# Kernel optimization log

Measured on AMD Instinct MI355X. Metric: run time of the kernel, lower is better.

## Reference

```python
import jax, jax.numpy as jnp
import numpy as np
from jax import lax

B, C, H, W = 8, 256, 64, 64
HEADS = 8
STRIDE = 2


def _grouped_conv(x, w, b, stride, groups):
    # x: [B, Cin, H, W]; w: [Cout, Cin/groups, k, k] (OIHW)
    y = lax.conv_general_dilated(x, w, (stride, stride), 'VALID',
                                 dimension_numbers=('NCHW', 'OIHW', 'NCHW'),
                                 feature_group_count=groups)
    return y + b[None, :, None, None]


def _grouped_conv_transpose(x, w, b, stride, groups):
    # Equivalent of torch ConvTranspose2d(kernel=stride, stride=stride, groups=groups)
    # implemented as lhs-dilated conv. w: [Cout, Cin/groups, k, k] (already in conv-equivalent layout).
    k = w.shape[-1]
    pad = k - 1
    y = lax.conv_general_dilated(x, w, (1, 1), [(pad, pad), (pad, pad)],
                                 lhs_dilation=(stride, stride),
                                 dimension_numbers=('NCHW', 'OIHW', 'NCHW'),
                                 feature_group_count=groups)
    return y + b[None, :, None, None]


def setup_inputs() -> dict:
    key = jax.random.key(0)
    ks = jax.random.split(key, 12)
    s = 0.05
    inp = {
        'q': jax.random.normal(ks[0], (B, C, H, W), jnp.float32),
        'k': jax.random.normal(ks[1], (B, C, H, W), jnp.float32),
        'v': jax.random.normal(ks[2], (B, C, H, W), jnp.float32),
        # grouped QKV conv weights: groups=C, out=C*HEADS -> [C*HEADS, 1, s, s]
        'wq': jax.random.normal(ks[3], (C * HEADS, 1, STRIDE, STRIDE), jnp.float32) * s,
        'bq': jax.random.normal(ks[4], (C * HEADS,), jnp.float32) * s,
        'wk': jax.random.normal(ks[5], (C * HEADS, 1, STRIDE, STRIDE), jnp.float32) * s,
        'bk': jax.random.normal(ks[6], (C * HEADS,), jnp.float32) * s,
        'wv': jax.random.normal(ks[7], (C * HEADS, 1, STRIDE, STRIDE), jnp.float32) * s,
        'bv': jax.random.normal(ks[8], (C * HEADS,), jnp.float32) * s,
        # deconv (groups=C, in=C*HEADS, out=C) in conv-equivalent OIHW layout: [C, HEADS, s, s]
        'wo': jax.random.normal(ks[9], (C, HEADS, STRIDE, STRIDE), jnp.float32) * s,
        'bo': jax.random.normal(ks[10], (C,), jnp.float32) * s,
        'gamma': jax.random.normal(ks[11], (1,), jnp.float32),
    }
    return inp


def reference(q, k, v, wq, bq, wk, bk, wv, bv, wo, bo, gamma):
    Bn, Cq, Hq, Wsp = q.shape
    Ckv = k.shape[1]
    # grouped conv projections -> [B, heads, C, L]
    pq = _grouped_conv(q, wq, bq, STRIDE, Cq).reshape(Bn, HEADS, Cq, -1)
    pk = _grouped_conv(k, wk, bk, STRIDE, Ckv).reshape(Bn, HEADS, Ckv, -1)
    pv = _grouped_conv(v, wv, bv, STRIDE, Ckv).reshape(Bn, HEADS, Ckv, -1)
    scale = pq.shape[3] ** (-0.5)
    # channel-wise attention: [B, h, Cq, Ckv]
    attn = jax.nn.softmax(jnp.einsum('bhcl,bhdl->bhcd', pq, pk) * scale, axis=-1)
    out = jnp.einsum('bhcd,bhdl->bhcl', attn, pv)  # [B, h, Cq, L]
    out = out.reshape(Bn, HEADS * Cq, Hq // STRIDE, Wsp // STRIDE)
    out = _grouped_conv_transpose(out, wo, bo, STRIDE, Cq)  # [B, Cq, Hq, Wsp]
    # dropout is identity at inference
    return q + out * gamma
```

## Files before the change

kernel.cpp:

```cpp
#include <hip/hip_runtime.h>
#include <hip/hip_bf16.h>

typedef __bf16 bf16;
typedef __bf16 bf16x4 __attribute__((ext_vector_type(4)));
typedef __bf16 bf16x8 __attribute__((ext_vector_type(8)));
typedef float f32x4 __attribute__((ext_vector_type(4)));

__device__ __forceinline__ void gload16(const void* g, void* l) {
  __builtin_amdgcn_global_load_lds(
      (const __attribute__((address_space(1))) unsigned int*)g,
      (__attribute__((address_space(3))) unsigned int*)l, 16, 0, 0);
}


__global__ __launch_bounds__(256) void proj_kqv(
    const float* __restrict__ kin, const float* __restrict__ qin,
    const float* __restrict__ vin,
    const float* __restrict__ wk, const float* __restrict__ bk,
    const float* __restrict__ wq, const float* __restrict__ bq,
    const float* __restrict__ wv, const float* __restrict__ bv,
    bf16* __restrict__ Pk, bf16* __restrict__ Pq, bf16* __restrict__ Vt) {
  int b = blockIdx.y;
  int x = blockIdx.x;
  int t = threadIdx.x;
  __shared__ float ch[4288];
  if (x < 512) {
    int g = x & 255;
    const float* in   = (x < 256) ? kin : qin;
    const float* w    = (x < 256) ? wk : wq;
    const float* bias = (x < 256) ? bk : bq;
    bf16* out         = (x < 256) ? Pk : Pq;
    {
      const float4* src = reinterpret_cast<const float4*>(in + ((size_t)b*256 + g)*4096);
      float4* dst4 = reinterpret_cast<float4*>(ch);
#pragma unroll
      for (int i = 0; i < 4; i++) dst4[t + i*256] = src[t + i*256];
    }
    int wave = t >> 6;
    int j = (t >> 3) & 7, n = t & 7;
    float4 wvv = reinterpret_cast<const float4*>(w)[g*8 + j];
    float bj = bias[g*8 + j];
    __syncthreads();
    int h = g >> 5;
    int c0 = (g & 31)*8;
    int bh = b*8 + h;
#pragma unroll
    for (int p = 0; p < 4; p++) {
      int kb = p*4 + wave;
      int m = kb*2 + (n >> 2);
      int n0 = (n & 3)*8;
      float rr0[16], rr1[16];
      const float4* R0 = reinterpret_cast<const float4*>(ch + (2*m)*64 + 2*n0);
      const float4* R1 = reinterpret_cast<const float4*>(ch + (2*m+1)*64 + 2*n0);
#pragma unroll
      for (int u = 0; u < 4; u++) {
        *reinterpret_cast<float4*>(rr0 + u*4) = R0[u];
        *reinterpret_cast<float4*>(rr1 + u*4) = R1[u];
      }
      bf16x8 o;
#pragma unroll
      for (int u = 0; u < 8; u++)
        o[u] = (bf16)(bj + wvv.x*rr0[2*u] + wvv.y*rr0[2*u+1] + wvv.z*rr1[2*u] + wvv.w*rr1[2*u+1]);
      size_t off = (((size_t)bh*16 + kb)*256 + c0 + j)*64 + (size_t)((n ^ j)*8);
      *reinterpret_cast<bf16x8*>(out + off) = o;
    }
  } else {
    int r = x - 512;
    int m = r & 31, h = r >> 5;
    {
      int seg = t >> 2, part = t & 3;
      int gl = seg >> 1, ky = seg & 1;
      const float* src = vin + (((size_t)b*256 + h*32 + gl)*64 + (2*m + ky))*64;
      float* drow = ch + (gl*2 + ky)*67;
#pragma unroll
      for (int i = 0; i < 4; i++) {
        float4 v = reinterpret_cast<const float4*>(src)[part + i*4];
        int x0 = (part + i*4)*4;
        drow[x0]=v.x; drow[x0+1]=v.y; drow[x0+2]=v.z; drow[x0+3]=v.w;
      }
    }
    int cgrp = t & 31, lgr = t >> 5;
    int c0 = cgrp*8;
    float4 wv8[8]; float bb8[8];
#pragma unroll
    for (int u = 0; u < 8; u++) {
      wv8[u] = reinterpret_cast<const float4*>(wv)[h*256 + c0 + u];
      bb8[u] = bv[h*256 + c0 + u];
    }
    __syncthreads();
    const float* r0 = ch + (cgrp*2 + 0)*67;
    const float* r1 = ch + (cgrp*2 + 1)*67;
    int bh = b*8 + h;
    bf16* base = Vt + ((size_t)bh*4 + (c0 >> 6))*1024*64;
    int colx = (c0 & 63) ^ (lgr << 3);
#pragma unroll
    for (int p = 0; p < 4; p++) {
      int n = p*8 + lgr;
      int l = m*32 + n;
      float c00 = r0[2*n], c01 = r0[2*n+1], c10 = r1[2*n], c11 = r1[2*n+1];
      bf16x8 o;
#pragma unroll
      for (int u = 0; u < 8; u++)
        o[u] = (bf16)(bb8[u] + wv8[u].x*c00 + wv8[u].y*c01 + wv8[u].z*c10 + wv8[u].w*c11);
      *reinterpret_cast<bf16x8*>(base + (size_t)l*64 + colx) = o;
    }
  }
}

__global__ __launch_bounds__(256, 2) void attn_qk(
    const bf16* __restrict__ Pq, const bf16* __restrict__ Pk,
    bf16* __restrict__ Pattn) {
  int raw = blockIdx.x;
  int idx = raw >> 3;
  int bh = (raw & 7)*8 + (idx >> 2);
  int cs = idx & 3;
  int t = threadIdx.x, wave = t >> 6, lane = t & 63, lg = lane >> 4, lr = lane & 15;
  __shared__ __attribute__((aligned(16))) char smem[81920];
  bf16* Kb0 = reinterpret_cast<bf16*>(smem);
  bf16* Kb1 = reinterpret_cast<bf16*>(smem + 32768);
  bf16* Qb0 = reinterpret_cast<bf16*>(smem + 65536);
  bf16* Qb1 = reinterpret_cast<bf16*>(smem + 73728);
  float (*red)[64] = reinterpret_cast<float (*)[64]>(smem + 65536);
  bf16* Pst = reinterpret_cast<bf16*>(smem);
  const char* Kbase = (const char*)Pk + (size_t)bh*524288 + wave*8192 + lane*16;
  const char* Qbase = (const char*)Pq + (size_t)bh*524288 + (size_t)cs*8192 + wave*2048 + lane*16;
  char* Kd0 = (char*)Kb0 + wave*8192;  char* Kd1 = (char*)Kb1 + wave*8192;
  char* Qd0 = (char*)Qb0 + wave*2048;  char* Qd1 = (char*)Qb1 + wave*2048;

#define STAGE(kb, K_, Q_) { \
    const char* kc = Kbase + (size_t)(kb)*32768; \
    _Pragma("unroll") \
    for (int i_ = 0; i_ < 8; i_++) gload16(kc + i_*1024, (K_) + i_*1024); \
    const char* qc = Qbase + (size_t)(kb)*32768; \
    gload16(qc, (Q_)); gload16(qc + 1024, (Q_) + 1024); }

  f32x4 acc[4][4];
#pragma unroll
  for (int i = 0; i < 4; i++)
#pragma unroll
    for (int j = 0; j < 4; j++) { f32x4 z = {0.f,0.f,0.f,0.f}; acc[i][j] = z; }

  STAGE(0, Kd0, Qd0);
#pragma unroll
  for (int kb = 0; kb < 16; kb++) {
    if (kb < 15) {
      if (kb & 1) { STAGE(kb+1, Kd0, Qd0); } else { STAGE(kb+1, Kd1, Qd1); }
      asm volatile("s_waitcnt vmcnt(10)" ::: "memory");
    } else {
      asm volatile("s_waitcnt vmcnt(0)" ::: "memory");
    }
    __builtin_amdgcn_s_barrier();
    __builtin_amdgcn_sched_barrier(0);
    const bf16* Kc = (kb & 1) ? Kb1 : Kb0;
    const bf16* Qc = (kb & 1) ? Qb1 : Qb0;
#pragma unroll
    for (int ks = 0; ks < 2; ks++) {
      int colx = (ks*32 + lg*8) ^ ((lr & 7) << 3);
      bf16x8 a[4];
#pragma unroll
      for (int mi = 0; mi < 4; mi++)
        a[mi] = *reinterpret_cast<const bf16x8*>(Qc + (mi*16 + lr)*64 + colx);
#pragma unroll
      for (int ni = 0; ni < 4; ni++) {
        bf16x8 bv2 = *reinterpret_cast<const bf16x8*>(Kc + (wave*64 + ni*16 + lr)*64 + colx);
#pragma unroll
        for (int mi = 0; mi < 4; mi++)
          acc[mi][ni] = __builtin_amdgcn_mfma_f32_16x16x32_bf16(a[mi], bv2, acc[mi][ni], 0, 0, 0);
      }
    }
    __builtin_amdgcn_s_barrier();
    __builtin_amdgcn_sched_barrier(0);
  }
#undef STAGE
  const float scale = 0.03125f;
  float sums[4][4];
#pragma unroll
  for (int mi = 0; mi < 4; mi++)
#pragma unroll
    for (int r = 0; r < 4; r++) {
      float mx = fmaxf(fmaxf(acc[mi][0][r], acc[mi][1][r]), fmaxf(acc[mi][2][r], acc[mi][3][r]));
#pragma unroll
      for (int off = 1; off < 16; off <<= 1) mx = fmaxf(mx, __shfl_xor(mx, off, 64));
      red[wave][mi*16 + lg*4 + r] = mx;
    }
  __syncthreads();
#pragma unroll
  for (int mi = 0; mi < 4; mi++)
#pragma unroll
    for (int r = 0; r < 4; r++) {
      int clr = mi*16 + lg*4 + r;
      float mx = fmaxf(fmaxf(red[0][clr], red[1][clr]), fmaxf(red[2][clr], red[3][clr]));
      float s = 0.f;
#pragma unroll
      for (int ni = 0; ni < 4; ni++) {
        float p = __expf(scale*(acc[mi][ni][r] - mx));
        acc[mi][ni][r] = p; s += p;
      }
#pragma unroll
      for (int off = 1; off < 16; off <<= 1) s += __shfl_xor(s, off, 64);
      sums[mi][r] = s;
    }
  __syncthreads();
#pragma unroll
  for (int mi = 0; mi < 4; mi++)
#pragma unroll
    for (int r = 0; r < 4; r++) red[wave][mi*16 + lg*4 + r] = sums[mi][r];
  __syncthreads();
#pragma unroll
  for (int mi = 0; mi < 4; mi++)
#pragma unroll
    for (int r = 0; r < 4; r++) {
      int clr = mi*16 + lg*4 + r;
      float iv = 1.f/(red[0][clr] + red[1][clr] + red[2][clr] + red[3][clr]);
#pragma unroll
      for (int ni = 0; ni < 4; ni++) {
        int dl = ni*16 + lr;
        Pst[wave*4096 + clr*64 + (dl ^ ((clr & 7) << 3))] = (bf16)(acc[mi][ni][r]*iv);
      }
    }
  __syncthreads();
  const uint4* ls = reinterpret_cast<const uint4*>(Pst);
#pragma unroll
  for (int i = 0; i < 8; i++) {
    int f = i*256 + t;
    int kb = f >> 9, rem = f & 511;
    char* dst = (char*)Pattn + ((size_t)(bh*4 + kb)*256 + cs*64)*128 + (size_t)rem*16;
    *reinterpret_cast<uint4*>(dst) = ls[f];
  }
}

__global__ __launch_bounds__(256, 4) void pv_deconv(const bf16* __restrict__ Pattn,
    const bf16* __restrict__ Vt, const float* __restrict__ qin,
    const float* __restrict__ wo, const float* __restrict__ bo,
    const float* __restrict__ gamma, float* __restrict__ outp) {
  int raw = blockIdx.x;
  int idx = raw >> 3;
  int pair = (raw & 7)*32 + (idx >> 2);
  int tb = idx & 3;
  int mb = pair & 3, bh = pair >> 2;
  int h = bh & 7, b = bh >> 3;
  int t = threadIdx.x, wave = t >> 6, lane = t & 63, lg = lane >> 4, lr = lane & 15;
  __shared__ __attribute__((aligned(16))) char smem[40960];
  bf16* Pl   = reinterpret_cast<bf16*>(smem);
  bf16* Vl   = reinterpret_cast<bf16*>(smem + 8192);
  bf16* OlT  = reinterpret_cast<bf16*>(smem);
  float* wo_s = reinterpret_cast<float*>(smem + 36864);
  float* bo_s = reinterpret_cast<float*>(smem + 37888);
  const char* Pbase = (const char*)Pattn + ((size_t)bh*4*256 + tb*64)*128;
  const char* Vbase = (const char*)Vt + ((size_t)bh*4*1024 + mb*256)*128;
  f32x4 acc[4][4];
#pragma unroll
  for (int i = 0; i < 4; i++)
#pragma unroll
    for (int j = 0; j < 4; j++) { f32x4 z = {0.f,0.f,0.f,0.f}; acc[i][j] = z; }
  for (int kb = 0; kb < 4; kb++) {
    __syncthreads();
    {
      const char* pc = Pbase + (size_t)kb*32768 + wave*2048 + lane*16;
      char* pl = (char*)Pl + wave*2048;
#pragma unroll
      for (int i = 0; i < 2; i++) gload16(pc + i*1024, pl + i*1024);
      const char* vc = Vbase + (size_t)kb*131072 + wave*8192 + lane*16;
      char* vl = (char*)Vl + wave*8192;
#pragma unroll
      for (int i = 0; i < 8; i++) gload16(vc + i*1024, vl + i*1024);
    }
    __syncthreads();
#pragma unroll
    for (int ks = 0; ks < 2; ks++) {
      int colx = (ks*32 + lg*8) ^ ((lr & 7) << 3);
      bf16x8 a[4];
#pragma unroll
      for (int mi = 0; mi < 4; mi++)
        a[mi] = *reinterpret_cast<const bf16x8*>(Pl + (mi*16 + lr)*64 + colx);
#pragma unroll
      for (int ni = 0; ni < 4; ni++) {
        bf16x8 bv2 = *reinterpret_cast<const bf16x8*>(Vl + (wave*64 + ni*16 + lr)*64 + colx);
#pragma unroll
        for (int mi = 0; mi < 4; mi++)
          acc[mi][ni] = __builtin_amdgcn_mfma_f32_16x16x32_bf16(a[mi], bv2, acc[mi][ni], 0, 0, 0);
      }
    }
  }
  __syncthreads();
#pragma unroll
  for (int mi = 0; mi < 4; mi++)
#pragma unroll
    for (int ni = 0; ni < 4; ni++) {
      int l = wave*64 + ni*16 + lr;
      int cb = mi*16 + lg*4;
      bf16x4 p;
      p[0] = (bf16)acc[mi][ni][0]; p[1] = (bf16)acc[mi][ni][1];
      p[2] = (bf16)acc[mi][ni][2]; p[3] = (bf16)acc[mi][ni][3];
      *reinterpret_cast<bf16x4*>(OlT + l*66 + cb) = p;
    }
  wo_s[t] = wo[((size_t)(h*32 + tb*8 + (t>>5)))*32 + (t & 31)];
  if (t < 8) bo_s[t] = bo[h*32 + tb*8 + t];
  __syncthreads();
  int xq = t & 15, b5 = (t >> 4) & 1, ct = t >> 5;
  float2 wp[8];
#pragma unroll
  for (int j = 0; j < 8; j++)
    wp[j] = *reinterpret_cast<const float2*>(wo_s + ct*32 + j*4 + (1 - b5)*2);
  float bias = bo_s[ct];
  float gm = gamma[0];
  int co = h*32 + tb*8 + ct;
#pragma unroll
  for (int it = 0; it < 8; it++) {
    int y = it*2 + b5;
    int ll0 = it*32 + xq*2;
    bf16x4 o00 = *reinterpret_cast<const bf16x4*>(OlT + ll0*66 + ct*8);
    bf16x4 o01 = *reinterpret_cast<const bf16x4*>(OlT + ll0*66 + ct*8 + 4);
    bf16x4 o10 = *reinterpret_cast<const bf16x4*>(OlT + (ll0+1)*66 + ct*8);
    bf16x4 o11 = *reinterpret_cast<const bf16x4*>(OlT + (ll0+1)*66 + ct*8 + 4);
    float v0 = bias, v1 = bias, v2 = bias, v3 = bias;
#pragma unroll
    for (int j = 0; j < 4; j++) {
      float f0 = (float)o00[j], f1 = (float)o01[j];
      v0 += f0*wp[j].y;   v1 += f0*wp[j].x;
      v0 += f1*wp[4+j].y; v1 += f1*wp[4+j].x;
      float g0 = (float)o10[j], g1 = (float)o11[j];
      v2 += g0*wp[j].y;   v3 += g0*wp[j].x;
      v2 += g1*wp[4+j].y; v3 += g1*wp[4+j].x;
    }
    size_t oi = (((size_t)b*256 + co)*64 + (mb*16 + y))*64 + xq*4;
    float4 qv = *reinterpret_cast<const float4*>(qin + oi);
    float4 ov;
    ov.x = qv.x + gm*v0; ov.y = qv.y + gm*v1;
    ov.z = qv.z + gm*v2; ov.w = qv.w + gm*v3;
    *reinterpret_cast<float4*>(outp + oi) = ov;
  }
}

extern "C" void kernel_launch(void* const* d_in, const int* in_sizes, int n_in,
                              void* d_out, int out_size, void* d_ws, size_t ws_size,
                              hipStream_t stream) {
  const float* q  = (const float*)d_in[0];
  const float* k  = (const float*)d_in[1];
  const float* v  = (const float*)d_in[2];
  const float* wq = (const float*)d_in[3];
  const float* bq = (const float*)d_in[4];
  const float* wk = (const float*)d_in[5];
  const float* bk = (const float*)d_in[6];
  const float* wv = (const float*)d_in[7];
  const float* bv = (const float*)d_in[8];
  const float* wo = (const float*)d_in[9];
  const float* bo = (const float*)d_in[10];
  const float* gamma = (const float*)d_in[11];
  float* out = (float*)d_out;

  char* ws = (char*)d_ws;
  bf16* Pk    = (bf16*)(ws);
  bf16* Vt    = (bf16*)(ws + 33554432);
  bf16* Pattn = (bf16*)(ws + 67108864);
  bf16* Pq    = (bf16*)(ws + 75497472);

  proj_kqv<<<dim3(768, 8), 256, 0, stream>>>(k, q, v, wk, bk, wq, bq, wv, bv, Pk, Pq, Vt);
  attn_qk <<<dim3(256), 256, 0, stream>>>(Pq, Pk, Pattn);
  pv_deconv<<<dim3(1024), 256, 0, stream>>>(Pattn, Vt, q, wo, bo, gamma, out);
}
```

Measured before the change: 81.79 us.

## Fuse Q projection into attention QK kernel, drop Pq intermediate buffer

```diff
diff --git a/kernel.cpp b/kernel.cpp
--- a/kernel.cpp
+++ b/kernel.cpp
@@ -13,33 +13,27 @@
 }
 
 
-__global__ __launch_bounds__(256) void proj_kqv(
-    const float* __restrict__ kin, const float* __restrict__ qin,
-    const float* __restrict__ vin,
+__global__ __launch_bounds__(256) void proj_kv(
+    const float* __restrict__ kin, const float* __restrict__ vin,
     const float* __restrict__ wk, const float* __restrict__ bk,
-    const float* __restrict__ wq, const float* __restrict__ bq,
     const float* __restrict__ wv, const float* __restrict__ bv,
-    bf16* __restrict__ Pk, bf16* __restrict__ Pq, bf16* __restrict__ Vt) {
+    bf16* __restrict__ Pk, bf16* __restrict__ Vt) {
   int b = blockIdx.y;
   int x = blockIdx.x;
   int t = threadIdx.x;
   __shared__ float ch[4288];
-  if (x < 512) {
-    int g = x & 255;
-    const float* in   = (x < 256) ? kin : qin;
-    const float* w    = (x < 256) ? wk : wq;
-    const float* bias = (x < 256) ? bk : bq;
-    bf16* out         = (x < 256) ? Pk : Pq;
+  if (x < 256) {
+    int g = x;
     {
-      const float4* src = reinterpret_cast<const float4*>(in + ((size_t)b*256 + g)*4096);
+      const float4* src = reinterpret_cast<const float4*>(kin + ((size_t)b*256 + g)*4096);
       float4* dst4 = reinterpret_cast<float4*>(ch);
 #pragma unroll
       for (int i = 0; i < 4; i++) dst4[t + i*256] = src[t + i*256];
     }
     int wave = t >> 6;
     int j = (t >> 3) & 7, n = t & 7;
-    float4 wvv = reinterpret_cast<const float4*>(w)[g*8 + j];
-    float bj = bias[g*8 + j];
+    float4 wvv = reinterpret_cast<const float4*>(wk)[g*8 + j];
+    float bj = bk[g*8 + j];
     __syncthreads();
     int h = g >> 5;
     int c0 = (g & 31)*8;
@@ -62,10 +56,10 @@
       for (int u = 0; u < 8; u++)
         o[u] = (bf16)(bj + wvv.x*rr0[2*u] + wvv.y*rr0[2*u+1] + wvv.z*rr1[2*u] + wvv.w*rr1[2*u+1]);
       size_t off = (((size_t)bh*16 + kb)*256 + c0 + j)*64 + (size_t)((n ^ j)*8);
-      *reinterpret_cast<bf16x8*>(out + off) = o;
+      *reinterpret_cast<bf16x8*>(Pk + off) = o;
     }
   } else {
-    int r = x - 512;
+    int r = x - 256;
     int m = r & 31, h = r >> 5;
     {
       int seg = t >> 2, part = t & 3;
@@ -107,13 +101,15 @@
   }
 }
 
-__global__ __launch_bounds__(256, 2) void attn_qk(
-    const bf16* __restrict__ Pq, const bf16* __restrict__ Pk,
+__global__ __launch_bounds__(256, 2) void attn_fused(
+    const float* __restrict__ qraw, const float* __restrict__ wq,
+    const float* __restrict__ bq, const bf16* __restrict__ Pk,
     bf16* __restrict__ Pattn) {
   int raw = blockIdx.x;
   int idx = raw >> 3;
   int bh = (raw & 7)*8 + (idx >> 2);
   int cs = idx & 3;
+  int b = bh >> 3, h = bh & 7;
   int t = threadIdx.x, wave = t >> 6, lane = t & 63, lg = lane >> 4, lr = lane & 15;
   __shared__ __attribute__((aligned(16))) char smem[81920];
   bf16* Kb0 = reinterpret_cast<bf16*>(smem);
@@ -123,31 +119,72 @@
   float (*red)[64] = reinterpret_cast<float (*)[64]>(smem + 65536);
   bf16* Pst = reinterpret_cast<bf16*>(smem);
   const char* Kbase = (const char*)Pk + (size_t)bh*524288 + wave*8192 + lane*16;
-  const char* Qbase = (const char*)Pq + (size_t)bh*524288 + (size_t)cs*8192 + wave*2048 + lane*16;
   char* Kd0 = (char*)Kb0 + wave*8192;  char* Kd1 = (char*)Kb1 + wave*8192;
-  char* Qd0 = (char*)Qb0 + wave*2048;  char* Qd1 = (char*)Qb1 + wave*2048;
-
-#define STAGE(kb, K_, Q_) { \
+
+  int gg = 2*wave + (lane >> 5);
+  int j  = (lane >> 2) & 7;
+  int nq = lane & 3;
+  int g  = h*32 + cs*8 + gg;
+  const float* qch = qraw + ((size_t)b*256 + g)*4096;
+  float4 wvq = reinterpret_cast<const float4*>(wq)[g*8 + j];
+  float bj = bq[g*8 + j];
+  int x0 = nq*16;
+  bf16x8 qreg[16][2];
+#pragma unroll
+  for (int kb = 0; kb < 16; kb++) {
+#pragma unroll
+    for (int half = 0; half < 2; half++) {
+      int y0 = kb*4 + half*2;
+      const float4* R0 = reinterpret_cast<const float4*>(qch + y0*64 + x0);
+      const float4* R1 = reinterpret_cast<const float4*>(qch + (y0+1)*64 + x0);
+      float f0[16], f1[16];
+#pragma unroll
+      for (int u = 0; u < 4; u++) {
+        *reinterpret_cast<float4*>(f0 + u*4) = R0[u];
+        *reinterpret_cast<float4*>(f1 + u*4) = R1[u];
+      }
+      bf16x8 o;
+#pragma unroll
+      for (int u = 0; u < 8; u++)
+        o[u] = (bf16)(bj + wvq.x*f0[2*u] + wvq.y*f0[2*u+1] + wvq.z*f1[2*u] + wvq.w*f1[2*u+1]);
+      qreg[kb][half] = o;
+    }
+  }
+  int qrow = gg*8 + j;
+  bf16* qw0a = Qb0 + qrow*64 + ((nq     ^ j)*8);
+  bf16* qw0b = Qb0 + qrow*64 + (((4+nq) ^ j)*8);
+  bf16* qw1a = Qb1 + qrow*64 + ((nq     ^ j)*8);
+  bf16* qw1b = Qb1 + qrow*64 + (((4+nq) ^ j)*8);
+
+#define STAGEK(kb, K_) { \
     const char* kc = Kbase + (size_t)(kb)*32768; \
     _Pragma("unroll") \
-    for (int i_ = 0; i_ < 8; i_++) gload16(kc + i_*1024, (K_) + i_*1024); \
-    const char* qc = Qbase + (size_t)(kb)*32768; \
-    gload16(qc, (Q_)); gload16(qc + 1024, (Q_) + 1024); }
+    for (int i_ = 0; i_ < 8; i_++) gload16(kc + i_*1024, (K_) + i_*1024); }
 
   f32x4 acc[4][4];
 #pragma unroll
   for (int i = 0; i < 4; i++)
 #pragma unroll
-    for (int j = 0; j < 4; j++) { f32x4 z = {0.f,0.f,0.f,0.f}; acc[i][j] = z; }
-
-  STAGE(0, Kd0, Qd0);
+    for (int jj = 0; jj < 4; jj++) { f32x4 z = {0.f,0.f,0.f,0.f}; acc[i][jj] = z; }
+
+  *reinterpret_cast<bf16x8*>(qw0a) = qreg[0][0];
+  *reinterpret_cast<bf16x8*>(qw0b) = qreg[0][1];
+  STAGEK(0, Kd0);
 #pragma unroll
   for (int kb = 0; kb < 16; kb++) {
     if (kb < 15) {
-      if (kb & 1) { STAGE(kb+1, Kd0, Qd0); } else { STAGE(kb+1, Kd1, Qd1); }
-      asm volatile("s_waitcnt vmcnt(10)" ::: "memory");
+      if (kb & 1) {
+        STAGEK(kb+1, Kd0);
+        *reinterpret_cast<bf16x8*>(qw0a) = qreg[kb+1][0];
+        *reinterpret_cast<bf16x8*>(qw0b) = qreg[kb+1][1];
+      } else {
+        STAGEK(kb+1, Kd1);
+        *reinterpret_cast<bf16x8*>(qw1a) = qreg[kb+1][0];
+        *reinterpret_cast<bf16x8*>(qw1b) = qreg[kb+1][1];
+      }
+      asm volatile("s_waitcnt vmcnt(8) lgkmcnt(0)" ::: "memory");
     } else {
-      asm volatile("s_waitcnt vmcnt(0)" ::: "memory");
+      asm volatile("s_waitcnt vmcnt(0) lgkmcnt(0)" ::: "memory");
     }
     __builtin_amdgcn_s_barrier();
     __builtin_amdgcn_sched_barrier(0);
@@ -171,7 +208,7 @@
     __builtin_amdgcn_s_barrier();
     __builtin_amdgcn_sched_barrier(0);
   }
-#undef STAGE
+#undef STAGEK
   const float scale = 0.03125f;
   float sums[4][4];
 #pragma unroll
@@ -353,9 +390,8 @@
   bf16* Pk    = (bf16*)(ws);
   bf16* Vt    = (bf16*)(ws + 33554432);
   bf16* Pattn = (bf16*)(ws + 67108864);
-  bf16* Pq    = (bf16*)(ws + 75497472);
-
-  proj_kqv<<<dim3(768, 8), 256, 0, stream>>>(k, q, v, wk, bk, wq, bq, wv, bv, Pk, Pq, Vt);
-  attn_qk <<<dim3(256), 256, 0, stream>>>(Pq, Pk, Pattn);
+
+  proj_kv  <<<dim3(512, 8), 256, 0, stream>>>(k, v, wk, bk, wv, bv, Pk, Vt);
+  attn_fused<<<dim3(256), 256, 0, stream>>>(q, wq, bq, Pk, Pattn);
   pv_deconv<<<dim3(1024), 256, 0, stream>>>(Pattn, Vt, q, wo, bo, gamma, out);
 }
```

After: 89.35 us. 1.09x slower.
